# Performance work log

Hardware: AMD Instinct MI355X
Metric: run time of the kernel (lower is better)

The kernel has to match this reference:

```python
import jax, jax.numpy as jnp
import numpy as np

N, IN, OUT, T = 500000, 128, 64, 8

def setup_inputs() -> dict:
    key = jax.random.key(0)
    k1, k2, k3, k4 = jax.random.split(key, 4)
    x = jax.random.normal(k1, (N, IN), dtype=jnp.float32)
    node_type = jax.random.randint(k2, (N,), 0, T, dtype=jnp.int32)
    # per-type Linear weights, stored as [T, IN, OUT] so x @ W[t] matches torch Linear
    W = jax.random.normal(k3, (T, IN, OUT), dtype=jnp.float32) * (1.0 / np.sqrt(IN))
    b = jax.random.normal(k4, (T, OUT), dtype=jnp.float32) * 0.01
    return {"x": x, "node_type": node_type, "W": W, "b": b}

def reference(x, node_type, W, b):
    # emb_x[mask_t] = x[mask_t] @ W[t] + b[t], for each node type t.
    # Vectorized: loop over the small fixed number of types, masked accumulate.
    T_ = W.shape[0]
    out = jnp.zeros((x.shape[0], W.shape[2]), dtype=x.dtype)
    for t in range(T_):
        y_t = x @ W[t] + b[t]                      # [N, OUT]
        mask = (node_type == t)[:, None]           # [N, 1]
        out = jnp.where(mask, y_t, out)
    return out
```

## Files before the change

kernel.cpp:

```cpp
#include <hip/hip_runtime.h>
#include <hip/hip_bf16.h>

#define NT   8
#define INF  128
#define OUTF 64
#define MT   4

typedef __attribute__((ext_vector_type(8))) short short8;
typedef __attribute__((ext_vector_type(4))) float f32x4;

__device__ __forceinline__ short f2bf(float f) {
  __hip_bfloat16 h = __float2bfloat16(f);
  return __builtin_bit_cast(short, h);
}

__global__ void hl_wconv(const float* __restrict__ W, short* __restrict__ wbf) {
  const int tid   = blockIdx.x * blockDim.x + threadIdx.x;
  const int combo = tid >> 6;
  const int lane  = tid & 63;
  const int t = combo >> 4, s = (combo >> 2) & 3, nb = combo & 3;
  const int q = lane >> 4, c = lane & 15;
  const float* Wt = W + t * INF * OUTF;
  short8 v;
  #pragma unroll
  for (int j = 0; j < 8; ++j)
    v[j] = f2bf(Wt[(s * 32 + q * 8 + j) * OUTF + nb * 16 + c]);
  *(short8*)(wbf + (size_t)tid * 8) = v;
}

__global__ __launch_bounds__(256, 2) void hl_main(
    const float* __restrict__ x, const int* __restrict__ nty,
    const short* __restrict__ wbf, const float* __restrict__ b,
    float* __restrict__ out, int N) {
  const int npass = (N + 63) >> 6;
  const int wave = threadIdx.x >> 6;
  const int lane = threadIdx.x & 63;
  const int q = lane >> 4, c = lane & 15;
  const int nwaves = gridDim.x * 4;
  const short* wp = wbf + (size_t)lane * 8;

  for (int pass = blockIdx.x * 4 + wave; pass < npass; pass += nwaves) {
    const int base = pass * 64;

    short8 A[MT][4];
    int tys[MT];
    #pragma unroll
    for (int i = 0; i < MT; ++i) {
      int rowa = base + i * 16 + c;
      if (rowa > N - 1) rowa = N - 1;
      tys[i] = nty[rowa];
      const float* xr = x + (size_t)rowa * INF;
      #pragma unroll
      for (int s = 0; s < 4; ++s) {
        f32x4 v0 = *(const f32x4*)(xr + s * 32 + q * 8);
        f32x4 v1 = *(const f32x4*)(xr + s * 32 + q * 8 + 4);
        short8 a;
        #pragma unroll
        for (int j = 0; j < 4; ++j) { a[j] = f2bf(v0[j]); a[j + 4] = f2bf(v1[j]); }
        A[i][s] = a;
      }
    }

    f32x4 acc[MT][4];
    #pragma unroll
    for (int i = 0; i < MT; ++i)
      #pragma unroll
      for (int nb = 0; nb < 4; ++nb) acc[i][nb] = (f32x4){0, 0, 0, 0};

    const short8 z8 = {0, 0, 0, 0, 0, 0, 0, 0};

    short8 BA[4], BB[4];
    #pragma unroll
    for (int nb = 0; nb < 4; ++nb) BA[nb] = *(const short8*)(wp + (size_t)nb * 512);

    #pragma unroll 1
    for (int t = 0; t < NT; ++t) {
      #pragma unroll
      for (int s = 0; s < 4; ++s) {
        const int g = t * 4 + s;
        const int gn = (g + 1 < 32) ? g + 1 : 31;
        if ((s & 1) == 0) {
          #pragma unroll
          for (int nb = 0; nb < 4; ++nb)
            BB[nb] = *(const short8*)(wp + (size_t)(gn * 4 + nb) * 512);
          #pragma unroll
          for (int i = 0; i < MT; ++i) {
            short8 am = (tys[i] == t) ? A[i][s] : z8;
            #pragma unroll
            for (int nb = 0; nb < 4; ++nb)
              acc[i][nb] = __builtin_amdgcn_mfma_f32_16x16x32_bf16(am, BA[nb], acc[i][nb], 0, 0, 0);
          }
        } else {
          #pragma unroll
          for (int nb = 0; nb < 4; ++nb)
            BA[nb] = *(const short8*)(wp + (size_t)(gn * 4 + nb) * 512);
          #pragma unroll
          for (int i = 0; i < MT; ++i) {
            short8 am = (tys[i] == t) ? A[i][s] : z8;
            #pragma unroll
            for (int nb = 0; nb < 4; ++nb)
              acc[i][nb] = __builtin_amdgcn_mfma_f32_16x16x32_bf16(am, BB[nb], acc[i][nb], 0, 0, 0);
          }
        }
      }
    }

    #pragma unroll
    for (int i = 0; i < MT; ++i) {
      const int rbase = base + i * 16 + q * 4;
      if (rbase >= N) continue;
      int4 tyv;
      if (rbase + 3 < N) {
        tyv = *(const int4*)(nty + rbase);
      } else {
        tyv.x = rbase + 0 < N ? nty[rbase + 0] : 0;
        tyv.y = rbase + 1 < N ? nty[rbase + 1] : 0;
        tyv.z = rbase + 2 < N ? nty[rbase + 2] : 0;
        tyv.w = rbase + 3 < N ? nty[rbase + 3] : 0;
      }
      const int trs[4] = {tyv.x, tyv.y, tyv.z, tyv.w};
      #pragma unroll
      for (int r = 0; r < 4; ++r) {
        const int row = rbase + r;
        if (row < N) {
          const float* br = b + trs[r] * OUTF + c;
          float* orow = out + (size_t)row * OUTF + c;
          #pragma unroll
          for (int nb = 0; nb < 4; ++nb)
            orow[nb * 16] = acc[i][nb][r] + br[nb * 16];
        }
      }
    }
  }
}

extern "C" void kernel_launch(void* const* d_in, const int* in_sizes, int n_in,
                              void* d_out, int out_size, void* d_ws, size_t ws_size,
                              hipStream_t stream) {
  const float* x  = (const float*)d_in[0];
  const int*   nt = (const int*)d_in[1];
  const float* W  = (const float*)d_in[2];
  const float* b  = (const float*)d_in[3];
  float* out = (float*)d_out;
  const int N = in_sizes[1];
  short* wbf = (short*)d_ws;

  hl_wconv<<<32, 256, 0, stream>>>(W, wbf);
  hl_main<<<512, 256, 0, stream>>>(x, nt, wbf, b, out, N);
}
```

Before: 428.3 us.

## Bucket rows by node type and run grouped GEMM instead of masked all-type MFMA

```diff
diff --git a/kernel.cpp b/kernel.cpp
--- a/kernel.cpp
+++ b/kernel.cpp
@@ -5,6 +5,7 @@
 #define INF  128
 #define OUTF 64
 #define MT   4
+#define MB   2
 
 typedef __attribute__((ext_vector_type(8))) short short8;
 typedef __attribute__((ext_vector_type(4))) float f32x4;
@@ -14,7 +15,8 @@
   return __builtin_bit_cast(short, h);
 }
 
-__global__ void hl_wconv(const float* __restrict__ W, short* __restrict__ wbf) {
+__global__ void hl_wconv(const float* __restrict__ W, short* __restrict__ wbf,
+                         int* __restrict__ cnt) {
   const int tid   = blockIdx.x * blockDim.x + threadIdx.x;
   const int combo = tid >> 6;
   const int lane  = tid & 63;
@@ -26,9 +28,156 @@
   for (int j = 0; j < 8; ++j)
     v[j] = f2bf(Wt[(s * 32 + q * 8 + j) * OUTF + nb * 16 + c]);
   *(short8*)(wbf + (size_t)tid * 8) = v;
-}
-
-__global__ __launch_bounds__(256, 2) void hl_main(
+  if (cnt && tid < NT) cnt[tid] = 0;
+}
+
+__global__ __launch_bounds__(256) void hl_hist(const int* __restrict__ nty, int N,
+                                               int* __restrict__ cnt) {
+  __shared__ int h[NT];
+  if (threadIdx.x < NT) h[threadIdx.x] = 0;
+  __syncthreads();
+  const int stride = gridDim.x * 1024;
+  for (int i0 = (blockIdx.x * 256 + threadIdx.x) * 4; i0 < N; i0 += stride) {
+    if (i0 + 3 < N) {
+      int4 v = *(const int4*)(nty + i0);
+      atomicAdd(&h[v.x], 1); atomicAdd(&h[v.y], 1);
+      atomicAdd(&h[v.z], 1); atomicAdd(&h[v.w], 1);
+    } else {
+      for (int k = i0; k < N; ++k) atomicAdd(&h[nty[k]], 1);
+    }
+  }
+  __syncthreads();
+  if (threadIdx.x < NT && h[threadIdx.x]) atomicAdd(&cnt[threadIdx.x], h[threadIdx.x]);
+}
+
+__global__ void hl_off(const int* __restrict__ cnt, int* __restrict__ poff,
+                       int* __restrict__ cursor, int* __restrict__ idx) {
+  __shared__ int sp[NT + 1], sc[NT];
+  if (threadIdx.x == 0) {
+    int o = 0;
+    for (int t = 0; t < NT; ++t) {
+      sp[t] = o; sc[t] = cnt[t];
+      o += (cnt[t] + 63) & ~63;
+      poff[t] = sp[t];
+      cursor[t] = sp[t];
+    }
+    sp[NT] = o;
+    poff[NT] = o;
+  }
+  __syncthreads();
+  for (int t = 0; t < NT; ++t)
+    for (int k = sp[t] + sc[t] + (int)threadIdx.x; k < sp[t + 1]; k += blockDim.x)
+      idx[k] = -1;
+}
+
+__global__ __launch_bounds__(256) void hl_scat(const int* __restrict__ nty, int N,
+                                               int* __restrict__ cursor,
+                                               int* __restrict__ idx) {
+  __shared__ int lbase[NT], lcnt[NT];
+  const int stride = gridDim.x * 1024;
+  for (int cb = blockIdx.x * 1024; cb < N; cb += stride) {
+    if (threadIdx.x < NT) lcnt[threadIdx.x] = 0;
+    __syncthreads();
+    const int i0 = cb + threadIdx.x * 4;
+    int t[4]; int nv = 0;
+    if (i0 + 3 < N) {
+      int4 v = *(const int4*)(nty + i0);
+      t[0] = v.x; t[1] = v.y; t[2] = v.z; t[3] = v.w; nv = 4;
+    } else {
+      for (int k = 0; k < 4 && i0 + k < N; ++k) { t[k] = nty[i0 + k]; ++nv; }
+    }
+    int lofs[4];
+    for (int k = 0; k < nv; ++k) lofs[k] = atomicAdd(&lcnt[t[k]], 1);
+    __syncthreads();
+    if (threadIdx.x < NT && lcnt[threadIdx.x] > 0)
+      lbase[threadIdx.x] = atomicAdd(&cursor[threadIdx.x], lcnt[threadIdx.x]);
+    __syncthreads();
+    for (int k = 0; k < nv; ++k) idx[lbase[t[k]] + lofs[k]] = i0 + k;
+    __syncthreads();
+  }
+}
+
+__global__ __launch_bounds__(256, 4) void hl_bgemm(
+    const float* __restrict__ x, const short* __restrict__ wbf,
+    const float* __restrict__ b, const int* __restrict__ idx,
+    const int* __restrict__ poff, float* __restrict__ out) {
+  const int wave = threadIdx.x >> 6;
+  const int lane = threadIdx.x & 63;
+  const int q = lane >> 4, c = lane & 15;
+  const short* wp = wbf + (size_t)lane * 8;
+
+  int p[NT + 1];
+  #pragma unroll
+  for (int t = 0; t <= NT; ++t) p[t] = poff[t];
+  const int npass = p[NT] >> 5;
+  const int nwaves = gridDim.x * 4;
+
+  for (int pass = blockIdx.x * 4 + wave; pass < npass; pass += nwaves) {
+    const int base = pass * 32;
+    int t = 0;
+    #pragma unroll
+    for (int k = 1; k < NT; ++k) t += (base >= p[k]);
+
+    int rows[MB];
+    #pragma unroll
+    for (int i = 0; i < MB; ++i) rows[i] = idx[base + i * 16 + c];
+
+    short8 A[MB][4];
+    #pragma unroll
+    for (int i = 0; i < MB; ++i) {
+      const int r = rows[i] < 0 ? 0 : rows[i];
+      const float* xr = x + (size_t)r * INF;
+      #pragma unroll
+      for (int s = 0; s < 4; ++s) {
+        f32x4 v0 = *(const f32x4*)(xr + s * 32 + q * 8);
+        f32x4 v1 = *(const f32x4*)(xr + s * 32 + q * 8 + 4);
+        short8 a;
+        #pragma unroll
+        for (int j = 0; j < 4; ++j) { a[j] = f2bf(v0[j]); a[j + 4] = f2bf(v1[j]); }
+        A[i][s] = a;
+      }
+    }
+
+    f32x4 acc[MB][4];
+    #pragma unroll
+    for (int i = 0; i < MB; ++i)
+      #pragma unroll
+      for (int nb = 0; nb < 4; ++nb) acc[i][nb] = (f32x4){0, 0, 0, 0};
+
+    #pragma unroll
+    for (int s = 0; s < 4; ++s) {
+      short8 B[4];
+      #pragma unroll
+      for (int nb = 0; nb < 4; ++nb)
+        B[nb] = *(const short8*)(wp + (size_t)(((t * 4 + s) * 4 + nb)) * 512);
+      #pragma unroll
+      for (int i = 0; i < MB; ++i)
+        #pragma unroll
+        for (int nb = 0; nb < 4; ++nb)
+          acc[i][nb] = __builtin_amdgcn_mfma_f32_16x16x32_bf16(A[i][s], B[nb], acc[i][nb], 0, 0, 0);
+    }
+
+    float bv[4];
+    #pragma unroll
+    for (int nb = 0; nb < 4; ++nb) bv[nb] = b[t * OUTF + nb * 16 + c];
+    #pragma unroll
+    for (int i = 0; i < MB; ++i) {
+      int4 iv = *(const int4*)(idx + base + i * 16 + q * 4);
+      const int rr[4] = {iv.x, iv.y, iv.z, iv.w};
+      #pragma unroll
+      for (int r = 0; r < 4; ++r) {
+        if (rr[r] >= 0) {
+          float* orow = out + (size_t)rr[r] * OUTF + c;
+          #pragma unroll
+          for (int nb = 0; nb < 4; ++nb)
+            orow[nb * 16] = acc[i][nb][r] + bv[nb];
+        }
+      }
+    }
+  }
+}
+
+__global__ __launch_bounds__(256, 2) void hl_main_masked(
     const float* __restrict__ x, const int* __restrict__ nty,
     const short* __restrict__ wbf, const float* __restrict__ b,
     float* __restrict__ out, int N) {
@@ -145,6 +294,28 @@
   const int N = in_sizes[1];
   short* wbf = (short*)d_ws;
 
-  hl_wconv<<<32, 256, 0, stream>>>(W, wbf);
-  hl_main<<<512, 256, 0, stream>>>(x, nt, wbf, b, out, N);
-}
+  const size_t need = 131072 + sizeof(int) * (size_t)(64 + N + 576);
+
+  if (ws_size >= need && N > 0) {
+    int* meta   = (int*)((char*)d_ws + 131072);
+    int* cnt    = meta;
+    int* poff   = meta + 8;
+    int* cursor = meta + 24;
+    int* idx    = meta + 64;
+
+    int hb = (N + 1023) / 1024;
+    if (hb > 2048) hb = 2048;
+
+    hl_wconv<<<32, 256, 0, stream>>>(W, wbf, cnt);
+    hl_hist<<<hb, 256, 0, stream>>>(nt, N, cnt);
+    hl_off<<<1, 64, 0, stream>>>(cnt, poff, cursor, idx);
+    hl_scat<<<hb, 256, 0, stream>>>(nt, N, cursor, idx);
+
+    const int npass_max = (((N + 63) & ~63) + NT * 64) / 32;
+    const int gb = (npass_max + 3) / 4;
+    hl_bgemm<<<gb, 256, 0, stream>>>(x, wbf, b, idx, poff, out);
+  } else {
+    hl_wconv<<<32, 256, 0, stream>>>(W, wbf, nullptr);
+    hl_main_masked<<<512, 256, 0, stream>>>(x, nt, wbf, b, out, N);
+  }
+}
```

New measurement: 422.4 us. Within noise of the previous version (-1.4%).

## Bucket rows by node type in LDS so each tile runs only its own type's GEMM

Applied to the files above, without the earlier changes.

```diff
diff --git a/kernel.cpp b/kernel.cpp
--- a/kernel.cpp
+++ b/kernel.cpp
@@ -4,9 +4,10 @@
 #define NT   8
 #define INF  128
 #define OUTF 64
-#define MT   4
+#define BR   128
 
 typedef __attribute__((ext_vector_type(8))) short short8;
+typedef __attribute__((ext_vector_type(4))) short short4v;
 typedef __attribute__((ext_vector_type(4))) float f32x4;
 
 __device__ __forceinline__ short f2bf(float f) {
@@ -28,107 +29,102 @@
   *(short8*)(wbf + (size_t)tid * 8) = v;
 }
 
-__global__ __launch_bounds__(256, 2) void hl_main(
+__global__ __launch_bounds__(256, 4) void hl_lb(
     const float* __restrict__ x, const int* __restrict__ nty,
     const short* __restrict__ wbf, const float* __restrict__ b,
     float* __restrict__ out, int N) {
-  const int npass = (N + 63) >> 6;
-  const int wave = threadIdx.x >> 6;
-  const int lane = threadIdx.x & 63;
+  __shared__ short xs[BR * 128];
+  __shared__ int lcnt[NT], cbase[NT];
+  __shared__ int lorder[BR];
+  __shared__ int descs[16];
+  __shared__ int ndesc;
+
+  const int tid   = threadIdx.x;
+  const int base  = blockIdx.x * BR;
+  const int nrows = min(BR, N - base);
+
+  if (tid < NT) lcnt[tid] = 0;
+  __syncthreads();
+
+  const int nf4 = nrows * 32;
+  for (int f4 = tid; f4 < nf4; f4 += 256) {
+    const int row = f4 >> 5, q4 = f4 & 31;
+    f32x4 v = *(const f32x4*)(x + (size_t)(base + row) * INF + q4 * 4);
+    short4v s4;
+    s4[0] = f2bf(v[0]); s4[1] = f2bf(v[1]);
+    s4[2] = f2bf(v[2]); s4[3] = f2bf(v[3]);
+    const int byt = (q4 * 8) ^ ((row & 7) << 4);
+    *(short4v*)((char*)xs + row * 256 + byt) = s4;
+  }
+
+  int myrank = 0, myty = 0;
+  if (tid < nrows) {
+    myty = nty[base + tid];
+    myrank = atomicAdd(&lcnt[myty], 1);
+  }
+  __syncthreads();
+
+  if (tid == 0) {
+    int o = 0, nd = 0;
+    #pragma unroll
+    for (int t = 0; t < NT; ++t) {
+      cbase[t] = o;
+      const int cn = lcnt[t];
+      for (int j = 0; j < cn; j += 16) {
+        const int valid = min(16, cn - j);
+        descs[nd++] = t | (valid << 3) | ((o + j) << 8);
+      }
+      o += cn;
+    }
+    ndesc = nd;
+  }
+  __syncthreads();
+  if (tid < nrows) lorder[cbase[myty] + myrank] = tid;
+  __syncthreads();
+
+  const int wave = tid >> 6, lane = tid & 63;
   const int q = lane >> 4, c = lane & 15;
-  const int nwaves = gridDim.x * 4;
-  const short* wp = wbf + (size_t)lane * 8;
+  const int nd = ndesc;
+  const short* wp = wbf + lane * 8;
 
-  for (int pass = blockIdx.x * 4 + wave; pass < npass; pass += nwaves) {
-    const int base = pass * 64;
+  for (int i = wave; i < nd; i += 4) {
+    const int d = descs[i];
+    const int t = d & 7, valid = (d >> 3) & 31, loff = d >> 8;
 
-    short8 A[MT][4];
-    int tys[MT];
+    const int am   = c < valid ? c : valid - 1;
+    const int lrow = lorder[loff + am];
+    const char* arow = (const char*)xs + lrow * 256;
+    const int sw = (lrow & 7) << 4;
+    short8 A[4];
     #pragma unroll
-    for (int i = 0; i < MT; ++i) {
-      int rowa = base + i * 16 + c;
-      if (rowa > N - 1) rowa = N - 1;
-      tys[i] = nty[rowa];
-      const float* xr = x + (size_t)rowa * INF;
+    for (int s = 0; s < 4; ++s)
+      A[s] = *(const short8*)(arow + ((s * 64 + q * 16) ^ sw));
+
+    f32x4 acc[4];
+    #pragma unroll
+    for (int nb = 0; nb < 4; ++nb) acc[nb] = (f32x4){0, 0, 0, 0};
+
+    #pragma unroll
+    for (int s = 0; s < 4; ++s) {
       #pragma unroll
-      for (int s = 0; s < 4; ++s) {
-        f32x4 v0 = *(const f32x4*)(xr + s * 32 + q * 8);
-        f32x4 v1 = *(const f32x4*)(xr + s * 32 + q * 8 + 4);
-        short8 a;
-        #pragma unroll
-        for (int j = 0; j < 4; ++j) { a[j] = f2bf(v0[j]); a[j + 4] = f2bf(v1[j]); }
-        A[i][s] = a;
+      for (int nb = 0; nb < 4; ++nb) {
+        short8 B = *(const short8*)(wp + (size_t)(((t * 4 + s) * 4 + nb)) * 512);
+        acc[nb] = __builtin_amdgcn_mfma_f32_16x16x32_bf16(A[s], B, acc[nb], 0, 0, 0);
       }
     }
 
-    f32x4 acc[MT][4];
+    float bv[4];
     #pragma unroll
-    for (int i = 0; i < MT; ++i)
-      #pragma unroll
-      for (int nb = 0; nb < 4; ++nb) acc[i][nb] = (f32x4){0, 0, 0, 0};
-
-    const short8 z8 = {0, 0, 0, 0, 0, 0, 0, 0};
-
-    short8 BA[4], BB[4];
+    for (int nb = 0; nb < 4; ++nb) bv[nb] = b[t * OUTF + nb * 16 + c];
     #pragma unroll
-    for (int nb = 0; nb < 4; ++nb) BA[nb] = *(const short8*)(wp + (size_t)nb * 512);
-
-    #pragma unroll 1
-    for (int t = 0; t < NT; ++t) {
-      #pragma unroll
-      for (int s = 0; s < 4; ++s) {
-        const int g = t * 4 + s;
-        const int gn = (g + 1 < 32) ? g + 1 : 31;
-        if ((s & 1) == 0) {
-          #pragma unroll
-          for (int nb = 0; nb < 4; ++nb)
-            BB[nb] = *(const short8*)(wp + (size_t)(gn * 4 + nb) * 512);
-          #pragma unroll
-          for (int i = 0; i < MT; ++i) {
-            short8 am = (tys[i] == t) ? A[i][s] : z8;
-            #pragma unroll
-            for (int nb = 0; nb < 4; ++nb)
-              acc[i][nb] = __builtin_amdgcn_mfma_f32_16x16x32_bf16(am, BA[nb], acc[i][nb], 0, 0, 0);
-          }
-        } else {
-          #pragma unroll
-          for (int nb = 0; nb < 4; ++nb)
-            BA[nb] = *(const short8*)(wp + (size_t)(gn * 4 + nb) * 512);
-          #pragma unroll
-          for (int i = 0; i < MT; ++i) {
-            short8 am = (tys[i] == t) ? A[i][s] : z8;
-            #pragma unroll
-            for (int nb = 0; nb < 4; ++nb)
-              acc[i][nb] = __builtin_amdgcn_mfma_f32_16x16x32_bf16(am, BB[nb], acc[i][nb], 0, 0, 0);
-          }
-        }
-      }
-    }
-
-    #pragma unroll
-    for (int i = 0; i < MT; ++i) {
-      const int rbase = base + i * 16 + q * 4;
-      if (rbase >= N) continue;
-      int4 tyv;
-      if (rbase + 3 < N) {
-        tyv = *(const int4*)(nty + rbase);
-      } else {
-        tyv.x = rbase + 0 < N ? nty[rbase + 0] : 0;
-        tyv.y = rbase + 1 < N ? nty[rbase + 1] : 0;
-        tyv.z = rbase + 2 < N ? nty[rbase + 2] : 0;
-        tyv.w = rbase + 3 < N ? nty[rbase + 3] : 0;
-      }
-      const int trs[4] = {tyv.x, tyv.y, tyv.z, tyv.w};
-      #pragma unroll
-      for (int r = 0; r < 4; ++r) {
-        const int row = rbase + r;
-        if (row < N) {
-          const float* br = b + trs[r] * OUTF + c;
-          float* orow = out + (size_t)row * OUTF + c;
-          #pragma unroll
-          for (int nb = 0; nb < 4; ++nb)
-            orow[nb * 16] = acc[i][nb][r] + br[nb * 16];
-        }
+    for (int r = 0; r < 4; ++r) {
+      const int m = q * 4 + r;
+      if (m < valid) {
+        const int grow = base + lorder[loff + m];
+        float* orow = out + (size_t)grow * OUTF + c;
+        #pragma unroll
+        for (int nb = 0; nb < 4; ++nb)
+          orow[nb * 16] = acc[nb][r] + bv[nb];
       }
     }
   }
@@ -146,5 +142,6 @@
   short* wbf = (short*)d_ws;
 
   hl_wconv<<<32, 256, 0, stream>>>(W, wbf);
-  hl_main<<<512, 256, 0, stream>>>(x, nt, wbf, b, out, N);
+  const int gb = (N + BR - 1) / BR;
+  hl_lb<<<gb, 256, 0, stream>>>(x, nt, wbf, b, out, N);
 }
```

Result: faster. 412.8 us (-3.6%).
